# Kernel tuning notes

Measured on AMD Instinct MI355X. Metric: run time of the kernel, lower is better.

The kernel has to match this reference:

```python
import jax, jax.numpy as jnp
import numpy as np

N, Q, E, D = 100000, 128, 500000, 32
D4 = 4 * D
RATIO_UPDATE = 0.2
NEG_SLOPE = 0.01  # LeakyReLU default


def setup_inputs() -> dict:
    key = jax.random.key(0)
    ks = jax.random.split(key, 16)
    return {
        "visited_node_score": jax.random.uniform(ks[0], (N,), jnp.float32),
        "node_repr": jax.random.normal(ks[1], (N, D), jnp.float32),
        "eg0": jnp.sort(jax.random.randint(ks[2], (E,), 0, Q)),
        "src0": jax.random.randint(ks[3], (E,), 0, N),
        "dst0": jax.random.randint(ks[4], (E,), 0, N),
        "rel0": jax.random.normal(ks[5], (E, D), jnp.float32),
        "eg1": jnp.sort(jax.random.randint(ks[6], (E,), 0, Q)),
        "src1": jax.random.randint(ks[7], (E,), 0, N),
        "dst1": jax.random.randint(ks[8], (E,), 0, N),
        "rel1": jax.random.normal(ks[9], (E, D), jnp.float32),
        "query_src_emb": jax.random.normal(ks[10], (Q, D), jnp.float32),
        "query_rel_emb": jax.random.normal(ks[11], (Q, D), jnp.float32),
        "Wq": jax.random.normal(ks[12], (D4, D4), jnp.float32) * np.sqrt(2.0 / D4).astype(np.float32),
        "Wk": jax.random.normal(ks[13], (D4, D4), jnp.float32) * np.sqrt(2.0 / D4).astype(np.float32),
        "Wlin": jax.random.normal(ks[14], (D, D), jnp.float32) * np.sqrt(2.0 / (2 * D)).astype(np.float32),
        "blin": jnp.zeros((D,), jnp.float32),
        "max_edges": 500,
    }


def segment_softmax(logits, seg, num_segments):
    # softmax within groups of identical seg id (source node index)
    m = jax.ops.segment_max(logits, seg, num_segments=num_segments)
    ex = jnp.exp(logits - m[seg])
    s = jax.ops.segment_sum(ex, seg, num_segments=num_segments)
    return ex / s[seg]


def segment_topk_mask(values, seg, k):
    # keep mask for per-segment top-k (seg must be sorted); stable -> first occurrence on ties
    n = values.shape[0]
    order = jnp.lexsort((-values, seg))  # primary: seg, secondary: descending value
    seg_sorted = seg[order]
    idx = jnp.arange(n)
    is_start = jnp.concatenate([jnp.array([True]), seg_sorted[1:] != seg_sorted[:-1]])
    seg_start = jax.lax.cummax(jnp.where(is_start, idx, 0))
    rank_sorted = idx - seg_start  # rank within segment, 0 = largest
    rank = jnp.zeros((n,), jnp.int32).at[order].set(rank_sorted.astype(jnp.int32))
    return rank < k


def reference(visited_node_score, node_repr, eg0, src0, dst0, rel0,
              eg1, src1, dst1, rel1, query_src_emb, query_rel_emb,
              Wq, Wk, Wlin, blin, max_edges):
    def att_logits(repr_, src, dst, eg, rel):
        q = query_src_emb[eg]
        r = query_rel_emb[eg]
        left = jnp.concatenate([repr_[src], rel, q, r], axis=-1)   # [E, 4D]
        right = jnp.concatenate([repr_[dst], rel, q, r], axis=-1)  # [E, 4D]
        return jnp.sum((left @ Wq.T) * (right @ Wk.T), axis=-1)    # [E]

    num_nodes = node_repr.shape[0]

    # ---- last layer: attention + segmented top-k pruning ----
    logits1 = att_logits(node_repr, src1, dst1, eg1, rel1)
    w1 = segment_softmax(logits1, src1, num_nodes)           # softmax over out-edges of each src node
    src_score = visited_node_score[src1]
    target_score = w1 * src_score
    keep = segment_topk_mask(target_score, eg1, max_edges)   # top-k per eg_idx
    w1p = jnp.where(keep, w1, 0.0)

    # node score aggregation == 'sum': score[n] = sum_{kept e: dst=n} w * src_score
    updated_node_score = jax.ops.segment_sum(w1p * src_score, dst1, num_segments=num_nodes)

    # representation update along pruned edges (linear_act=False)
    agg = jax.ops.segment_sum(w1p[:, None] * node_repr[src1], dst1, num_segments=num_nodes)
    repr_ = (1.0 - RATIO_UPDATE) * agg + RATIO_UPDATE * node_repr

    # ---- earlier layer(s), no pruning ----
    logits0 = att_logits(repr_, src0, dst0, eg0, rel0)
    w0 = segment_softmax(logits0, src0, num_nodes)
    agg0 = jax.ops.segment_sum(w0[:, None] * repr_[src0], dst0, num_segments=num_nodes)
    repr_ = (1.0 - RATIO_UPDATE) * agg0 + RATIO_UPDATE * repr_

    # bypass_forward: LeakyReLU(Linear(repr))
    h = repr_ @ Wlin.T + blin
    updated_repr = jnp.where(h >= 0, h, NEG_SLOPE * h)
    return updated_node_score, updated_repr
```

## Files before the change

kernel.cpp:

```cpp
#include <hip/hip_runtime.h>
#include <math.h>

#define DD 32
#define DD4 128
#define TPB 256
#define LDSCAP 6144
#define CANDCAP 2048

__device__ __forceinline__ unsigned long long dsort_key(double x) {
  unsigned long long b = (unsigned long long)__double_as_longlong(x);
  return (b & 0x8000000000000000ull) ? ~b : (b | 0x8000000000000000ull);
}
__device__ __forceinline__ double dunsort_key(unsigned long long k) {
  unsigned long long b = (k & 0x8000000000000000ull) ? (k ^ 0x8000000000000000ull) : ~k;
  return __longlong_as_double((long long)b);
}
__device__ __forceinline__ unsigned int fsort_key(float x) {
  unsigned int b = __float_as_uint(x);
  return (b & 0x80000000u) ? ~b : (b | 0x80000000u);
}
__device__ __forceinline__ float funsort_key(unsigned int k) {
  unsigned int b = (k & 0x80000000u) ? (k ^ 0x80000000u) : ~k;
  return __uint_as_float(b);
}

__device__ __forceinline__ int block_iscan256(int x, int* wsum) {
  const int lane = threadIdx.x & 63, w = threadIdx.x >> 6;
#pragma unroll
  for (int o = 1; o < 64; o <<= 1) {
    int y = __shfl_up(x, o, 64);
    if (lane >= o) x += y;
  }
  if (lane == 63) wsum[w] = x;
  __syncthreads();
  int add = 0;
#pragma unroll
  for (int i = 0; i < 4; ++i) add += (i < w) ? wsum[i] : 0;
  __syncthreads();
  return x + add;
}

__global__ __launch_bounds__(TPB) void k_precompute_M(
    const float* __restrict__ Wq, const float* __restrict__ Wk,
    double* __restrict__ M64) {
  int t = blockIdx.x * blockDim.x + threadIdx.x;
  int i = t >> 7, j = t & 127;
  double acc = 0.0;
  for (int k = 0; k < DD4; ++k)
    acc += (double)Wq[k * DD4 + i] * (double)Wk[k * DD4 + j];
  M64[i * DD4 + j] = acc;
}

__global__ __launch_bounds__(64) void k_per_query(
    const double* __restrict__ M64,
    const float* __restrict__ qemb, const float* __restrict__ remb,
    double* __restrict__ p64, double* __restrict__ pD64, double* __restrict__ c64,
    float* __restrict__ p32, float* __restrict__ pD32, float* __restrict__ c32) {
  int q = blockIdx.x;
  int l = threadIdx.x;
  __shared__ double qr[64];
  qr[l] = (l < DD) ? (double)qemb[q * DD + l] : (double)remb[q * DD + (l - DD)];
  __syncthreads();
  double a = 0.0;
  for (int j = 0; j < 64; ++j) a += M64[l * DD4 + 64 + j] * qr[j];
  double ct = 0.0;
  for (int j = 0; j < 64; ++j) ct += M64[(64 + j) * DD4 + l] * qr[j];
  if (l >= DD) a += ct;
  p64[q * 64 + l] = a;
  p32[q * 64 + l] = (float)a;
  if (l < DD) {
    pD64[q * DD + l] = ct;
    pD32[q * DD + l] = (float)ct;
  }
  double a3 = 0.0;
  for (int j = 0; j < 64; ++j) a3 += M64[(64 + l) * DD4 + 64 + j] * qr[j];
  a3 *= qr[l];
  for (int o = 32; o; o >>= 1) a3 += __shfl_xor(a3, o);
  if (l == 0) { c64[q] = a3; c32[q] = (float)a3; }
}

template <typename T, bool MIX>
__global__ __launch_bounds__(TPB) void k_node_pre(
    const double* __restrict__ M64, const float* __restrict__ reprIn,
    const float* __restrict__ aggIn, float* __restrict__ reprOut,
    float* __restrict__ t, float* __restrict__ u, float* __restrict__ v, int N_) {
  __shared__ T G11s[32 * 32];
  __shared__ T G12Ts[32 * 32];
  __shared__ T G21s[32 * 32];
  for (int i = threadIdx.x; i < 1024; i += TPB) {
    int r = i >> 5, c = i & 31;
    G11s[i]  = (T)M64[r * DD4 + c];
    G12Ts[i] = (T)M64[c * DD4 + 32 + r];
    G21s[i]  = (T)M64[(32 + r) * DD4 + c];
  }
  __syncthreads();
  int n = blockIdx.x * TPB + threadIdx.x;
  if (n >= N_) return;
  float h[32];
  const float4* h4 = (const float4*)reprIn + (size_t)n * 8;
  if constexpr (MIX) {
    const float4* a4 = (const float4*)aggIn + (size_t)n * 8;
    float4* o4 = (float4*)reprOut + (size_t)n * 8;
#pragma unroll
    for (int j = 0; j < 8; ++j) {
      float4 x = h4[j], y = a4[j];
      float4 m = make_float4(0.8f * y.x + 0.2f * x.x, 0.8f * y.y + 0.2f * x.y,
                             0.8f * y.z + 0.2f * x.z, 0.8f * y.w + 0.2f * x.w);
      o4[j] = m;
      h[4 * j] = m.x; h[4 * j + 1] = m.y; h[4 * j + 2] = m.z; h[4 * j + 3] = m.w;
    }
  } else {
#pragma unroll
    for (int j = 0; j < 8; ++j) {
      float4 x = h4[j];
      h[4 * j] = x.x; h[4 * j + 1] = x.y; h[4 * j + 2] = x.z; h[4 * j + 3] = x.w;
    }
  }
  float4* t4 = (float4*)t + (size_t)n * 8;
  float4* u4 = (float4*)u + (size_t)n * 8;
  float4* v4 = (float4*)v + (size_t)n * 8;
#pragma unroll
  for (int ig = 0; ig < 8; ++ig) {
    float to[4], uo[4], vo[4];
#pragma unroll
    for (int ii = 0; ii < 4; ++ii) {
      const int i = ig * 4 + ii;
      T at = (T)0, au = (T)0, av = (T)0;
#pragma unroll
      for (int j = 0; j < 32; ++j) {
        T hj = (T)h[j];
        at += G11s[i * 32 + j] * hj;
        au += G12Ts[i * 32 + j] * hj;
        av += G21s[i * 32 + j] * hj;
      }
      to[ii] = (float)at; uo[ii] = (float)au; vo[ii] = (float)av;
    }
    t4[ig] = make_float4(to[0], to[1], to[2], to[3]);
    u4[ig] = make_float4(uo[0], uo[1], uo[2], uo[3]);
    v4[ig] = make_float4(vo[0], vo[1], vo[2], vo[3]);
  }
}

template <typename T>
__global__ __launch_bounds__(TPB) void k_quad(
    const double* __restrict__ M64,
    const float* __restrict__ rel, const int* __restrict__ eg,
    const T* __restrict__ pq, const T* __restrict__ cq,
    T* __restrict__ quad, int E) {
  __shared__ T G22s[32 * 32];
  for (int i = threadIdx.x; i < 1024; i += TPB) {
    int r = i >> 5, c = i & 31;
    G22s[i] = (T)M64[(32 + r) * DD4 + 32 + c];
  }
  __syncthreads();
  const int e = blockIdx.x * TPB + threadIdx.x;
  if (e >= E) return;
  const int q = eg[e];
  T rl[32];
  {
    const float4* r4 = (const float4*)rel + (size_t)e * 8;
#pragma unroll
    for (int j = 0; j < 8; ++j) {
      float4 x = r4[j];
      rl[4 * j] = (T)x.x; rl[4 * j + 1] = (T)x.y;
      rl[4 * j + 2] = (T)x.z; rl[4 * j + 3] = (T)x.w;
    }
  }
  const T* prow = pq + (size_t)q * 64 + 32;
  T acc0 = cq[q], acc1 = (T)0;
#pragma unroll
  for (int i = 0; i < 32; ++i) {
    T r0 = prow[i], r1 = (T)0;
#pragma unroll
    for (int j = 0; j < 32; j += 2) {
      r0 += G22s[i * 32 + j] * rl[j];
      r1 += G22s[i * 32 + j + 1] * rl[j + 1];
    }
    if (i & 1) acc1 += rl[i] * (r0 + r1);
    else       acc0 += rl[i] * (r0 + r1);
  }
  quad[e] = acc0 + acc1;
}

template <typename T>
__global__ __launch_bounds__(TPB) void k_edge_dots(
    const float* __restrict__ repr, const float* __restrict__ rel,
    const int* __restrict__ src, const int* __restrict__ dst, const int* __restrict__ eg,
    const float* __restrict__ tvec, const float* __restrict__ uvec, const float* __restrict__ vvec,
    const T* __restrict__ pq, const T* __restrict__ pDq, const T* __restrict__ quad,
    T* __restrict__ logits, void* __restrict__ mkey, int E) {
  const long long t = (long long)blockIdx.x * TPB + threadIdx.x;
  const int e = (int)(t >> 3), part = (int)(t & 7);
  if (e >= E) return;
  const int s = src[e], d = dst[e], q = eg[e];
  const float4 hs = ((const float4*)repr)[(size_t)s * 8 + part];
  const float4 td = ((const float4*)tvec)[(size_t)d * 8 + part];
  const float4 hd = ((const float4*)repr)[(size_t)d * 8 + part];
  const float4 rl = ((const float4*)rel)[(size_t)e * 8 + part];
  const float4 us = ((const float4*)uvec)[(size_t)s * 8 + part];
  const float4 vd = ((const float4*)vvec)[(size_t)d * 8 + part];
  const T* p  = pq  + (size_t)q * 64 + part * 4;
  const T* pD = pDq + (size_t)q * DD + part * 4;
  T a = (T)hs.x * ((T)td.x + p[0]) + (T)hs.y * ((T)td.y + p[1]) +
        (T)hs.z * ((T)td.z + p[2]) + (T)hs.w * ((T)td.w + p[3]);
  a += (T)hd.x * pD[0] + (T)hd.y * pD[1] + (T)hd.z * pD[2] + (T)hd.w * pD[3];
  a += (T)rl.x * (T)(us.x + vd.x) + (T)rl.y * (T)(us.y + vd.y) +
       (T)rl.z * (T)(us.z + vd.z) + (T)rl.w * (T)(us.w + vd.w);
  a += __shfl_xor(a, 1);
  a += __shfl_xor(a, 2);
  a += __shfl_xor(a, 4);
  if (part == 0) {
    a += quad[e];
    logits[e] = a;
    if constexpr (sizeof(T) == 8) {
      atomicMax((unsigned long long*)mkey + s, dsort_key((double)a));
    } else {
      atomicMax((unsigned int*)mkey + s, fsort_key((float)a));
    }
  }
}

__global__ __launch_bounds__(TPB) void k_expsum64(
    double* __restrict__ io, const unsigned long long* __restrict__ mkey,
    const int* __restrict__ src, double* __restrict__ ssum, int E) {
  int e = blockIdx.x * blockDim.x + threadIdx.x;
  if (e >= E) return;
  int s = src[e];
  double ex = exp(io[e] - dunsort_key(mkey[s]));
  io[e] = ex;
  atomicAdd(&ssum[s], ex);
}
__global__ __launch_bounds__(TPB) void k_expsum32h(
    float* __restrict__ io, const unsigned int* __restrict__ mkey,
    const int* __restrict__ src, const int* __restrict__ dst,
    float* __restrict__ ssum, int* __restrict__ cnt, int E) {
  int e = blockIdx.x * blockDim.x + threadIdx.x;
  if (e >= E) return;
  int s = src[e];
  float ex = expf(io[e] - funsort_key(mkey[s]));
  io[e] = ex;
  atomicAdd(&ssum[s], ex);
  atomicAdd(&cnt[dst[e]], 1);
}

__global__ __launch_bounds__(TPB) void k_weights_target(
    const double* __restrict__ ex, const double* __restrict__ ssum,
    const int* __restrict__ src, const float* __restrict__ score,
    const int* __restrict__ eg, int* __restrict__ qoff,
    float* __restrict__ w1f, unsigned int* __restrict__ tkey, int E, int Q) {
  int e = blockIdx.x * blockDim.x + threadIdx.x;
  if (e >= E) return;
  int s = src[e];
  double w = ex[e] / ssum[s];
  float wf = (float)w;
  w1f[e] = wf;
  float tgt = wf * score[s];
  tkey[e] = fsort_key(tgt);
  int cur = eg[e];
  int prev = (e == 0) ? -1 : eg[e - 1];
  for (int v = prev + 1; v <= cur; ++v) qoff[v] = e;
  if (e == E - 1) {
    for (int v = cur + 1; v <= Q; ++v) qoff[v] = E;
  }
}

__global__ __launch_bounds__(TPB) void k_topk(
    const unsigned int* __restrict__ tkey, const float* __restrict__ w1f,
    const int* __restrict__ qoff, const int* __restrict__ maxe,
    float* __restrict__ w1p, int E) {
  __shared__ unsigned int keys[LDSCAP];
  __shared__ int hist[256];
  __shared__ unsigned short cand[CANDCAP];
  __shared__ int wsum[4];
  __shared__ int sh_cnt;
  __shared__ unsigned int sh_prefix;
  __shared__ int sh_need;
  const int q = blockIdx.x;
  const int s = qoff[q], e2 = qoff[q + 1];
  const int n = e2 - s;
  const int K = maxe[0];
  if (n <= K) {
    for (int i = s + threadIdx.x; i < e2; i += TPB) w1p[i] = w1f[i];
    return;
  }
  const bool useLds = (n <= LDSCAP);
  if (useLds) {
    for (int i = threadIdx.x; i < n; i += TPB) keys[i] = tkey[s + i];
  }
  hist[threadIdx.x] = 0;
  __syncthreads();
  for (int i = threadIdx.x; i < n; i += TPB) {
    unsigned int k = useLds ? keys[i] : tkey[s + i];
    atomicAdd(&hist[k >> 24], 1);
  }
  __syncthreads();
  int need = K;
  {
    int h = hist[255 - threadIdx.x];
    int incl = block_iscan256(h, wsum);
    int excl = incl - h;
    if (incl >= need && excl < need) {
      sh_prefix = (unsigned int)(255 - threadIdx.x) << 24;
      sh_need = need - excl;
    }
  }
  __syncthreads();
  unsigned int prefix = sh_prefix;
  need = sh_need;
  const int cnt0 = hist[prefix >> 24];
  const bool compact = useLds && (cnt0 <= CANDCAP);
  if (threadIdx.x == 0) sh_cnt = 0;
  __syncthreads();
  if (compact) {
    const unsigned int d0 = prefix >> 24;
    for (int i = threadIdx.x; i < n; i += TPB) {
      if ((keys[i] >> 24) == d0) {
        int p = atomicAdd(&sh_cnt, 1);
        cand[p] = (unsigned short)i;
      }
    }
  }
  __syncthreads();
  const int ncand = compact ? sh_cnt : 0;
  for (int pass = 1; pass < 4; ++pass) {
    const int shift = 24 - 8 * pass;
    const unsigned int himask = 0xFFFFFFFFu << (shift + 8);
    hist[threadIdx.x] = 0;
    __syncthreads();
    if (compact) {
      for (int ci = threadIdx.x; ci < ncand; ci += TPB) {
        unsigned int k = keys[cand[ci]];
        if ((k & himask) == prefix) atomicAdd(&hist[(k >> shift) & 255], 1);
      }
    } else {
      for (int i = threadIdx.x; i < n; i += TPB) {
        unsigned int k = useLds ? keys[i] : tkey[s + i];
        if ((k & himask) == prefix) atomicAdd(&hist[(k >> shift) & 255], 1);
      }
    }
    __syncthreads();
    int h = hist[255 - threadIdx.x];
    int incl = block_iscan256(h, wsum);
    int excl = incl - h;
    if (incl >= need && excl < need) {
      sh_prefix = prefix | ((unsigned int)(255 - threadIdx.x) << shift);
      sh_need = need - excl;
    }
    __syncthreads();
    prefix = sh_prefix;
    need = sh_need;
    __syncthreads();
  }
  const unsigned int kth = prefix;
  const int r = need;
  const int C = (n + TPB - 1) / TPB;
  const int b0 = min(threadIdx.x * C, n);
  const int b1 = min(b0 + C, n);
  int myt = 0;
  for (int i = b0; i < b1; ++i) {
    unsigned int k = useLds ? keys[i] : tkey[s + i];
    myt += (k == kth) ? 1 : 0;
  }
  int tincl = block_iscan256(myt, wsum);
  int tiepre = tincl - myt;
  for (int i = b0; i < b1; ++i) {
    unsigned int k = useLds ? keys[i] : tkey[s + i];
    float v = 0.f;
    if (k > kth) {
      v = w1f[s + i];
    } else if (k == kth) {
      if (tiepre < r) v = w1f[s + i];
      ++tiepre;
    }
    w1p[s + i] = v;
  }
}

__global__ __launch_bounds__(TPB) void k_apply1(
    const float* __restrict__ w1p, const int* __restrict__ src, const int* __restrict__ dst,
    const float* __restrict__ repr0, const float* __restrict__ score,
    float* __restrict__ agg, float* __restrict__ score_out, int E) {
  int t = blockIdx.x * blockDim.x + threadIdx.x;
  int e = t >> 3, part = t & 7;
  if (e >= E) return;
  float w = w1p[e];
  if (w == 0.f) return;
  int sv = src[e], dv = dst[e];
  const float4 rv = ((const float4*)repr0)[sv * 8 + part];
  float* ap = agg + (size_t)dv * DD + part * 4;
  atomicAdd(ap + 0, w * rv.x);
  atomicAdd(ap + 1, w * rv.y);
  atomicAdd(ap + 2, w * rv.z);
  atomicAdd(ap + 3, w * rv.w);
  if (part == 0) atomicAdd(score_out + dv, w * score[sv]);
}

#define SCHUNK 1024
__global__ __launch_bounds__(TPB) void k_scan1(
    const int* __restrict__ cnt, int* __restrict__ off, int* __restrict__ bsum, int N_) {
  __shared__ int sd[TPB];
  const int b = blockIdx.x, t = threadIdx.x;
  const int base = b * SCHUNK + t * 4;
  int v[4];
  int s4 = 0;
#pragma unroll
  for (int k = 0; k < 4; ++k) {
    v[k] = (base + k < N_) ? cnt[base + k] : 0;
    s4 += v[k];
  }
  sd[t] = s4;
  __syncthreads();
  for (int o = 1; o < TPB; o <<= 1) {
    int x = (t >= o) ? sd[t - o] : 0;
    __syncthreads();
    sd[t] += x;
    __syncthreads();
  }
  int excl = sd[t] - s4;
  if (t == TPB - 1) bsum[b] = sd[t];
  int run = excl;
#pragma unroll
  for (int k = 0; k < 4; ++k) {
    if (base + k < N_) { off[base + k] = run; run += v[k]; }
  }
}

__global__ __launch_bounds__(TPB) void k_scan2(
    int* __restrict__ bsum, int* __restrict__ off, int nblk, int N_, int E) {
  __shared__ int wsum[4];
  if (nblk <= TPB) {
    int t = threadIdx.x;
    int x = (t < nblk) ? bsum[t] : 0;
    int orig = x;
    const int lane = t & 63, w = t >> 6;
#pragma unroll
    for (int o = 1; o < 64; o <<= 1) {
      int y = __shfl_up(x, o, 64);
      if (lane >= o) x += y;
    }
    if (lane == 63) wsum[w] = x;
    __syncthreads();
    int add = 0;
#pragma unroll
    for (int i = 0; i < 4; ++i) add += (i < w) ? wsum[i] : 0;
    x += add;
    if (t < nblk) bsum[t] = x - orig;
    if (t == 0) off[N_] = E;
  } else {
    if (threadIdx.x != 0) return;
    int run = 0;
    for (int i = 0; i < nblk; ++i) { int tmp = bsum[i]; bsum[i] = run; run += tmp; }
    off[N_] = E;
  }
}

__global__ __launch_bounds__(TPB) void k_scan3(
    int* __restrict__ off, const int* __restrict__ bsum, int* __restrict__ cursor, int N_) {
  int i = blockIdx.x * blockDim.x + threadIdx.x;
  if (i >= N_) return;
  int v = off[i] + bsum[i >> 10];
  off[i] = v;
  cursor[i] = v;
}

__global__ __launch_bounds__(TPB) void k_scatter0(
    const float* __restrict__ ex, const float* __restrict__ ssum,
    const int* __restrict__ src, const int* __restrict__ dst,
    int* __restrict__ cursor, float2* __restrict__ pk, int E) {
  int e = blockIdx.x * blockDim.x + threadIdx.x;
  if (e >= E) return;
  int s = src[e];
  float w = ex[e] / ssum[s];
  int pos = atomicAdd(&cursor[dst[e]], 1);
  pk[pos] = make_float2(w, __int_as_float(s));
}

__global__ __launch_bounds__(TPB) void k_gather_final(
    const float2* __restrict__ pk, const int* __restrict__ off,
    const float* __restrict__ repr1,
    const float* __restrict__ Wlin, const float* __restrict__ blin,
    float* __restrict__ out_repr, int N_) {
  __shared__ float WsT[DD * DD];
  __shared__ float bs[DD];
  for (int i = threadIdx.x; i < DD * DD; i += TPB) {
    int r = i >> 5, c = i & 31;
    WsT[c * DD + r] = Wlin[i];
  }
  if (threadIdx.x < DD) bs[threadIdx.x] = blin[threadIdx.x];
  __syncthreads();
  const int n = blockIdx.x * 8 + (threadIdx.x >> 5);
  const int c = threadIdx.x & 31;
  if (n >= N_) return;
  float acc = 0.f;
  const int j1 = off[n + 1];
  for (int j = off[n]; j < j1; ++j) {
    float2 p = pk[j];
    int s = __float_as_int(p.y);
    acc += p.x * repr1[(size_t)s * DD + c];
  }
  float mix = 0.8f * acc + 0.2f * repr1[(size_t)n * DD + c];
  float o = bs[c];
#pragma unroll 8
  for (int j = 0; j < DD; ++j) {
    float mj = __shfl(mix, j, 32);
    o += WsT[j * DD + c] * mj;
  }
  out_repr[(size_t)n * DD + c] = (o >= 0.f) ? o : 0.01f * o;
}

extern "C" void kernel_launch(void* const* d_in, const int* in_sizes, int n_in,
                              void* d_out, int out_size, void* d_ws, size_t ws_size,
                              hipStream_t stream) {
  (void)n_in; (void)out_size; (void)ws_size;
  const float* score = (const float*)d_in[0];
  const float* nrepr = (const float*)d_in[1];
  const int*   eg0   = (const int*)d_in[2];
  const int*   src0  = (const int*)d_in[3];
  const int*   dst0  = (const int*)d_in[4];
  const float* rel0  = (const float*)d_in[5];
  const int*   eg1   = (const int*)d_in[6];
  const int*   src1  = (const int*)d_in[7];
  const int*   dst1  = (const int*)d_in[8];
  const float* rel1  = (const float*)d_in[9];
  const float* qemb  = (const float*)d_in[10];
  const float* remb  = (const float*)d_in[11];
  const float* Wq    = (const float*)d_in[12];
  const float* Wk    = (const float*)d_in[13];
  const float* Wlin  = (const float*)d_in[14];
  const float* blin  = (const float*)d_in[15];
  const int*   maxe  = (const int*)d_in[16];

  const int N_ = in_sizes[0];
  const int E_ = in_sizes[2];
  const int Q_ = in_sizes[10] / DD;

  char* wsc = (char*)d_ws;
  size_t off = 0;
  auto alloc = [&](size_t bytes) -> void* {
    void* p = wsc + off;
    off += (bytes + 255) & ~(size_t)255;
    return p;
  };
  double* M64  = (double*)alloc((size_t)DD4 * DD4 * 8);
  double* p64  = (double*)alloc((size_t)Q_ * 64 * 8);
  double* pD64 = (double*)alloc((size_t)Q_ * DD * 8);
  double* c64  = (double*)alloc((size_t)Q_ * 8);
  float*  p32  = (float*)alloc((size_t)Q_ * 64 * 4);
  float*  pD32 = (float*)alloc((size_t)Q_ * DD * 4);
  float*  c32  = (float*)alloc((size_t)Q_ * 4);
  int*    qoff = (int*)alloc((size_t)(Q_ + 2) * 4);
  double* lg1  = (double*)alloc((size_t)E_ * 8);
  double* qv64 = (double*)alloc((size_t)E_ * 8);
  float*  w1f  = (float*)alloc((size_t)E_ * 4);
  unsigned int* tkey = (unsigned int*)alloc((size_t)E_ * 4);
  float*  w1p  = (float*)alloc((size_t)E_ * 4);
  float*  lg0  = (float*)alloc((size_t)E_ * 4);
  float*  repr1 = (float*)alloc((size_t)N_ * DD * 4);
  float*  tvec = (float*)alloc((size_t)N_ * DD * 4);
  float*  uvec = (float*)alloc((size_t)N_ * DD * 4);
  float*  vvec = (float*)alloc((size_t)N_ * DD * 4);
  size_t zstart = off;
  unsigned long long* mkey1 = (unsigned long long*)alloc((size_t)N_ * 8);
  double* s1   = (double*)alloc((size_t)N_ * 8);
  float*  agg  = (float*)alloc((size_t)N_ * DD * 4);
  unsigned int* mkey0 = (unsigned int*)alloc((size_t)N_ * 4);
  float*  s0   = (float*)alloc((size_t)N_ * 4);
  size_t zlen = off - zstart;

  float* qv32 = (float*)qv64;

  int* cnt    = (int*)tvec;
  int* offcsr = (int*)tvec + N_;
  int* cursor = (int*)tvec + 2 * (size_t)N_ + 64;
  int* bsum   = (int*)tvec + 3 * (size_t)N_ + 128;
  float2* pk  = (float2*)uvec;

  float* out_score = (float*)d_out;
  float* out_repr  = out_score + N_;

  hipMemsetAsync(wsc + zstart, 0, zlen, stream);
  hipMemsetAsync(d_out, 0, (size_t)N_ * 4, stream);

  k_precompute_M<<<(DD4 * DD4) / TPB, TPB, 0, stream>>>(Wq, Wk, M64);
  k_per_query<<<Q_, 64, 0, stream>>>(M64, qemb, remb, p64, pD64, c64, p32, pD32, c32);

  const int ngrid = (N_ + TPB - 1) / TPB;
  const int egrid = (E_ + TPB - 1) / TPB;
  const int dgrid = (int)(((size_t)E_ * 8 + TPB - 1) / TPB);

  k_node_pre<double, false><<<ngrid, TPB, 0, stream>>>(M64, nrepr, nullptr, nullptr,
                                                       tvec, uvec, vvec, N_);
  k_quad<double><<<egrid, TPB, 0, stream>>>(M64, rel1, eg1, p64, c64, qv64, E_);
  k_edge_dots<double><<<dgrid, TPB, 0, stream>>>(nrepr, rel1, src1, dst1, eg1,
                                                 tvec, uvec, vvec, p64, pD64, qv64,
                                                 lg1, (void*)mkey1, E_);
  k_expsum64<<<egrid, TPB, 0, stream>>>(lg1, mkey1, src1, s1, E_);
  k_weights_target<<<egrid, TPB, 0, stream>>>(lg1, s1, src1, score, eg1, qoff,
                                              w1f, tkey, E_, Q_);
  k_topk<<<Q_, TPB, 0, stream>>>(tkey, w1f, qoff, maxe, w1p, E_);

  k_apply1<<<dgrid, TPB, 0, stream>>>(w1p, src1, dst1, nrepr, score, agg, out_score, E_);

  k_node_pre<float, true><<<ngrid, TPB, 0, stream>>>(M64, nrepr, agg, repr1,
                                                     tvec, uvec, vvec, N_);
  k_quad<float><<<egrid, TPB, 0, stream>>>(M64, rel0, eg0, p32, c32, qv32, E_);
  k_edge_dots<float><<<dgrid, TPB, 0, stream>>>(repr1, rel0, src0, dst0, eg0,
                                                tvec, uvec, vvec, p32, pD32, qv32,
                                                lg0, (void*)mkey0, E_);

  hipMemsetAsync(cnt, 0, (size_t)N_ * 4, stream);
  k_expsum32h<<<egrid, TPB, 0, stream>>>(lg0, mkey0, src0, dst0, s0, cnt, E_);
  const int nblk = (N_ + SCHUNK - 1) / SCHUNK;
  k_scan1<<<nblk, TPB, 0, stream>>>(cnt, offcsr, bsum, N_);
  k_scan2<<<1, TPB, 0, stream>>>(bsum, offcsr, nblk, N_, E_);
  k_scan3<<<ngrid, TPB, 0, stream>>>(offcsr, bsum, cursor, N_);
  k_scatter0<<<egrid, TPB, 0, stream>>>(lg0, s0, src0, dst0, cursor, pk, E_);
  k_gather_final<<<(N_ + 7) / 8, TPB, 0, stream>>>(pk, offcsr, repr1, Wlin, blin, out_repr, N_);
}
```

Before: 734.9 us.

## Symmetrize quadratic form in k_quad and remap node_pre to lane-per-feature

```diff
diff --git a/kernel.cpp b/kernel.cpp
--- a/kernel.cpp
+++ b/kernel.cpp
@@ -49,6 +49,15 @@
   for (int k = 0; k < DD4; ++k)
     acc += (double)Wq[k * DD4 + i] * (double)Wk[k * DD4 + j];
   M64[i * DD4 + j] = acc;
+}
+
+__global__ __launch_bounds__(TPB) void k_sym22(
+    const double* __restrict__ M64, double* __restrict__ S64) {
+  int i = blockIdx.x * blockDim.x + threadIdx.x;
+  int r = i >> 5, c = i & 31;
+  double g  = M64[(32 + r) * DD4 + 32 + c];
+  double gt = M64[(32 + c) * DD4 + 32 + r];
+  S64[i] = (c > r) ? (g + gt) : ((c == r) ? g : 0.0);
 }
 
 __global__ __launch_bounds__(64) void k_per_query(
@@ -84,74 +93,49 @@
     const double* __restrict__ M64, const float* __restrict__ reprIn,
     const float* __restrict__ aggIn, float* __restrict__ reprOut,
     float* __restrict__ t, float* __restrict__ u, float* __restrict__ v, int N_) {
-  __shared__ T G11s[32 * 32];
-  __shared__ T G12Ts[32 * 32];
-  __shared__ T G21s[32 * 32];
+  __shared__ T GT[3 * 32 * 32];
   for (int i = threadIdx.x; i < 1024; i += TPB) {
-    int r = i >> 5, c = i & 31;
-    G11s[i]  = (T)M64[r * DD4 + c];
-    G12Ts[i] = (T)M64[c * DD4 + 32 + r];
-    G21s[i]  = (T)M64[(32 + r) * DD4 + c];
-  }
-  __syncthreads();
-  int n = blockIdx.x * TPB + threadIdx.x;
-  if (n >= N_) return;
-  float h[32];
-  const float4* h4 = (const float4*)reprIn + (size_t)n * 8;
-  if constexpr (MIX) {
-    const float4* a4 = (const float4*)aggIn + (size_t)n * 8;
-    float4* o4 = (float4*)reprOut + (size_t)n * 8;
-#pragma unroll
-    for (int j = 0; j < 8; ++j) {
-      float4 x = h4[j], y = a4[j];
-      float4 m = make_float4(0.8f * y.x + 0.2f * x.x, 0.8f * y.y + 0.2f * x.y,
-                             0.8f * y.z + 0.2f * x.z, 0.8f * y.w + 0.2f * x.w);
-      o4[j] = m;
-      h[4 * j] = m.x; h[4 * j + 1] = m.y; h[4 * j + 2] = m.z; h[4 * j + 3] = m.w;
-    }
-  } else {
-#pragma unroll
-    for (int j = 0; j < 8; ++j) {
-      float4 x = h4[j];
-      h[4 * j] = x.x; h[4 * j + 1] = x.y; h[4 * j + 2] = x.z; h[4 * j + 3] = x.w;
-    }
-  }
-  float4* t4 = (float4*)t + (size_t)n * 8;
-  float4* u4 = (float4*)u + (size_t)n * 8;
-  float4* v4 = (float4*)v + (size_t)n * 8;
-#pragma unroll
-  for (int ig = 0; ig < 8; ++ig) {
-    float to[4], uo[4], vo[4];
-#pragma unroll
-    for (int ii = 0; ii < 4; ++ii) {
-      const int i = ig * 4 + ii;
-      T at = (T)0, au = (T)0, av = (T)0;
-#pragma unroll
-      for (int j = 0; j < 32; ++j) {
-        T hj = (T)h[j];
-        at += G11s[i * 32 + j] * hj;
-        au += G12Ts[i * 32 + j] * hj;
-        av += G21s[i * 32 + j] * hj;
-      }
-      to[ii] = (float)at; uo[ii] = (float)au; vo[ii] = (float)av;
-    }
-    t4[ig] = make_float4(to[0], to[1], to[2], to[3]);
-    u4[ig] = make_float4(uo[0], uo[1], uo[2], uo[3]);
-    v4[ig] = make_float4(vo[0], vo[1], vo[2], vo[3]);
+    int j = i >> 5, c = i & 31;
+    GT[i]        = (T)M64[c * DD4 + j];
+    GT[1024 + i] = (T)M64[j * DD4 + 32 + c];
+    GT[2048 + i] = (T)M64[(32 + c) * DD4 + j];
+  }
+  __syncthreads();
+  const int base = blockIdx.x * 32;
+  const int sub = threadIdx.x >> 5;
+  const int c = threadIdx.x & 31;
+#pragma unroll
+  for (int m = 0; m < 4; ++m) {
+    const int n = base + m * 8 + sub;
+    if (n >= N_) continue;
+    float h = reprIn[(size_t)n * DD + c];
+    if constexpr (MIX) {
+      float a = aggIn[(size_t)n * DD + c];
+      h = 0.8f * a + 0.2f * h;
+      reprOut[(size_t)n * DD + c] = h;
+    }
+    T ta = (T)0, ua = (T)0, va = (T)0;
+#pragma unroll
+    for (int j = 0; j < 32; ++j) {
+      T hj = (T)__shfl(h, j, 32);
+      ta += GT[j * 32 + c] * hj;
+      ua += GT[1024 + j * 32 + c] * hj;
+      va += GT[2048 + j * 32 + c] * hj;
+    }
+    t[(size_t)n * DD + c] = (float)ta;
+    u[(size_t)n * DD + c] = (float)ua;
+    v[(size_t)n * DD + c] = (float)va;
   }
 }
 
 template <typename T>
 __global__ __launch_bounds__(TPB) void k_quad(
-    const double* __restrict__ M64,
+    const double* __restrict__ S64,
     const float* __restrict__ rel, const int* __restrict__ eg,
     const T* __restrict__ pq, const T* __restrict__ cq,
     T* __restrict__ quad, int E) {
-  __shared__ T G22s[32 * 32];
-  for (int i = threadIdx.x; i < 1024; i += TPB) {
-    int r = i >> 5, c = i & 31;
-    G22s[i] = (T)M64[(32 + r) * DD4 + 32 + c];
-  }
+  __shared__ T Ss[32 * 32];
+  for (int i = threadIdx.x; i < 1024; i += TPB) Ss[i] = (T)S64[i];
   __syncthreads();
   const int e = blockIdx.x * TPB + threadIdx.x;
   if (e >= E) return;
@@ -167,19 +151,29 @@
     }
   }
   const T* prow = pq + (size_t)q * 64 + 32;
-  T acc0 = cq[q], acc1 = (T)0;
+  T lin0 = (T)0, lin1 = (T)0;
+#pragma unroll
+  for (int i = 0; i < 32; i += 2) {
+    lin0 += prow[i] * rl[i];
+    lin1 += prow[i + 1] * rl[i + 1];
+  }
+  T a0 = cq[q] + lin0, a1 = lin1, a2 = (T)0, a3 = (T)0;
 #pragma unroll
   for (int i = 0; i < 32; ++i) {
-    T r0 = prow[i], r1 = (T)0;
-#pragma unroll
-    for (int j = 0; j < 32; j += 2) {
-      r0 += G22s[i * 32 + j] * rl[j];
-      r1 += G22s[i * 32 + j + 1] * rl[j + 1];
-    }
-    if (i & 1) acc1 += rl[i] * (r0 + r1);
-    else       acc0 += rl[i] * (r0 + r1);
-  }
-  quad[e] = acc0 + acc1;
+    T r0 = Ss[i * 32 + i] * rl[i];
+    T r1 = (T)0;
+#pragma unroll
+    for (int j = i + 1; j < 32; ++j) {
+      if ((j - i) & 1) r1 += Ss[i * 32 + j] * rl[j];
+      else             r0 += Ss[i * 32 + j] * rl[j];
+    }
+    T rr = (r0 + r1) * rl[i];
+    if ((i & 3) == 0) a0 += rr;
+    else if ((i & 3) == 1) a1 += rr;
+    else if ((i & 3) == 2) a2 += rr;
+    else a3 += rr;
+  }
+  quad[e] = (a0 + a1) + (a2 + a3);
 }
 
 template <typename T>
@@ -542,6 +536,7 @@
     return p;
   };
   double* M64  = (double*)alloc((size_t)DD4 * DD4 * 8);
+  double* S64  = (double*)alloc((size_t)DD * DD * 8);
   double* p64  = (double*)alloc((size_t)Q_ * 64 * 8);
   double* pD64 = (double*)alloc((size_t)Q_ * DD * 8);
   double* c64  = (double*)alloc((size_t)Q_ * 8);
@@ -582,15 +577,17 @@
   hipMemsetAsync(d_out, 0, (size_t)N_ * 4, stream);
 
   k_precompute_M<<<(DD4 * DD4) / TPB, TPB, 0, stream>>>(Wq, Wk, M64);
+  k_sym22<<<4, TPB, 0, stream>>>(M64, S64);
   k_per_query<<<Q_, 64, 0, stream>>>(M64, qemb, remb, p64, pD64, c64, p32, pD32, c32);
 
   const int ngrid = (N_ + TPB - 1) / TPB;
+  const int n32grid = (N_ + 31) / 32;
   const int egrid = (E_ + TPB - 1) / TPB;
   const int dgrid = (int)(((size_t)E_ * 8 + TPB - 1) / TPB);
 
-  k_node_pre<double, false><<<ngrid, TPB, 0, stream>>>(M64, nrepr, nullptr, nullptr,
-                                                       tvec, uvec, vvec, N_);
-  k_quad<double><<<egrid, TPB, 0, stream>>>(M64, rel1, eg1, p64, c64, qv64, E_);
+  k_node_pre<double, false><<<n32grid, TPB, 0, stream>>>(M64, nrepr, nullptr, nullptr,
+                                                         tvec, uvec, vvec, N_);
+  k_quad<double><<<egrid, TPB, 0, stream>>>(S64, rel1, eg1, p64, c64, qv64, E_);
   k_edge_dots<double><<<dgrid, TPB, 0, stream>>>(nrepr, rel1, src1, dst1, eg1,
                                                  tvec, uvec, vvec, p64, pD64, qv64,
                                                  lg1, (void*)mkey1, E_);
@@ -601,9 +598,9 @@
 
   k_apply1<<<dgrid, TPB, 0, stream>>>(w1p, src1, dst1, nrepr, score, agg, out_score, E_);
 
-  k_node_pre<float, true><<<ngrid, TPB, 0, stream>>>(M64, nrepr, agg, repr1,
-                                                     tvec, uvec, vvec, N_);
-  k_quad<float><<<egrid, TPB, 0, stream>>>(M64, rel0, eg0, p32, c32, qv32, E_);
+  k_node_pre<float, true><<<n32grid, TPB, 0, stream>>>(M64, nrepr, agg, repr1,
+                                                       tvec, uvec, vvec, N_);
+  k_quad<float><<<egrid, TPB, 0, stream>>>(S64, rel0, eg0, p32, c32, qv32, E_);
   k_edge_dots<float><<<dgrid, TPB, 0, stream>>>(repr1, rel0, src0, dst0, eg0,
                                                 tvec, uvec, vvec, p32, pD32, qv32,
                                                 lg0, (void*)mkey0, E_);
```

Measured after the change: 688.5 us. -6.3%, faster.
